# Kernel optimization log

Hardware: AMD Instinct MI355X
Metric: run time of the kernel (lower is better)

## Reference

```python
import jax, jax.numpy as jnp
import numpy as np

B = 64
HIST_LEN, PRED_HORIZON = 10, 10
H = W = 200
RES = 0.1
INIT_X_IDX, INIT_Y_IDX = 100.0, 160.0
FRONT_EDGE, BACK_EDGE = 3.89, 1.043
HALF_BOX = (FRONT_EDGE + BACK_EDGE) / 2.0
CENTER_SHIFT = HALF_BOX - BACK_EDGE          # mid-circle shift along box heading
FRONT_SHIFT = 2.0 * HALF_BOX - 2.0 * BACK_EDGE
EMBED, HIDDEN, CNN_OUT, CNN_CH = 64, 128, 1000, 32
SIGMA = 1.8
THETA = 0.0


def setup_inputs() -> dict:
    key = jax.random.key(0)
    ks = jax.random.split(key, 16)
    def rn(k, shape, scale=0.02):
        return jax.random.normal(k, shape, dtype=jnp.float32) * scale
    return {
        "img_feature": jax.random.normal(ks[0], (B, 12, H, W), dtype=jnp.float32),
        "hist_points": rn(ks[1], (B, HIST_LEN, 4), 1.0),
        "hist_points_step": rn(ks[2], (B, HIST_LEN, 4), 0.1),
        "ego_rendering_heading": jax.random.uniform(ks[3], (B, 1), dtype=jnp.float32, maxval=2.0 * np.pi),
        "comp_w": rn(ks[4], (3, 12, 3, 3)),
        "comp_b": jnp.zeros((3,), jnp.float32),
        "cnn_w": rn(ks[5], (CNN_CH, 3, 3, 3)),
        "cnn_b": jnp.zeros((CNN_CH,), jnp.float32),
        "cnn_fc_w": rn(ks[6], (CNN_OUT, CNN_CH)),
        "cnn_fc_b": jnp.zeros((CNN_OUT,), jnp.float32),
        "embed_w": rn(ks[7], (EMBED, 4)),
        "embed_b": jnp.zeros((EMBED,), jnp.float32),
        "h0": rn(ks[8], (1, HIDDEN)),
        "c0": rn(ks[9], (1, HIDDEN)),
        "w_ih": rn(ks[10], (4 * HIDDEN, EMBED)),
        "w_hh": rn(ks[11], (4 * HIDDEN, HIDDEN)),
        "b_ih": jnp.zeros((4 * HIDDEN,), jnp.float32),
        "b_hh": jnp.zeros((4 * HIDDEN,), jnp.float32),
        "out_w": rn(ks[12], (4, HIDDEN + CNN_OUT)),
        "out_b": jnp.zeros((4,), jnp.float32),
    }


def _conv(x, w, b, stride):
    y = jax.lax.conv_general_dilated(x, w, (stride, stride), 'SAME',
                                     dimension_numbers=('NCHW', 'OIHW', 'NCHW'))
    return y + b[None, :, None, None]


def _forward(img_feature, hist_points, hist_points_step, ego_rendering_heading,
             comp_w, comp_b, cnn_w, cnn_b, cnn_fc_w, cnn_fc_b,
             embed_w, embed_b, h0, c0, w_ih, w_hh, b_ih, b_hh, out_w, out_b):
    bsz = img_feature.shape[0]
    # CNN encoder: 12->3 compression conv, then backbone (stand-in for mobilenet_v2) -> 1000-dim
    z = _conv(img_feature, comp_w, comp_b, 1)
    z = jax.nn.relu(_conv(z, cnn_w, cnn_b, 2))
    z = z.mean(axis=(2, 3))                       # (B, CNN_CH) global avg pool
    img_emb = z @ cnn_fc_w.T + cnn_fc_b           # (B, 1000)

    def lstm_cell(e, h, c):                       # pytorch gate order i, f, g, o
        g = e @ w_ih.T + b_ih + h @ w_hh.T + b_hh
        i, f, gg, o = jnp.split(g, 4, axis=-1)
        c2 = jax.nn.sigmoid(f) * c + jax.nn.sigmoid(i) * jnp.tanh(gg)
        return jax.nn.sigmoid(o) * jnp.tanh(c2), c2

    def embed(step):
        return jax.nn.relu(step @ embed_w.T + embed_b)

    h = jnp.tile(h0, (bsz, 1))
    c = jnp.tile(c0, (bsz, 1))

    # warm up LSTM on history displacements (torch loop t = 1 .. HIST_LEN-1)
    def hist_step(carry, step_t):
        h, c = carry
        h, c = lstm_cell(embed(step_t), h, c)
        return (h, c), None
    (h, c), _ = jax.lax.scan(hist_step, (h, c),
                             jnp.swapaxes(hist_points_step[:, 1:HIST_LEN], 0, 1))

    def pred_step(carry, _):
        h, c, pose = carry
        step = jnp.concatenate([h, img_emb], axis=1) @ out_w.T + out_b
        pose = pose + step
        h, c = lstm_cell(embed(step), h, c)
        return (h, c, pose), pose
    _, poses = jax.lax.scan(pred_step, (h, c, hist_points[:, HIST_LEN - 1]),
                            None, length=PRED_HORIZON)
    pred_traj = jnp.swapaxes(poses, 0, 1)         # (B, T, 4) == torch pred_traj[:, 1:, :]

    # three-circle gaussian rasterization, vectorized over all timesteps
    ego = ego_rendering_heading.reshape(bsz)      # (B,)
    x, y, hd = pred_traj[..., 0], pred_traj[..., 1], pred_traj[..., 2]
    box_heading = -hd - ego[:, None]              # (B, T)
    ho = -(ego - np.pi / 2.0)                     # heading_offset, (B,)
    cos_ho, sin_ho = jnp.cos(ho)[:, None], jnp.sin(ho)[:, None]
    px = INIT_X_IDX + (x * cos_ho - y * sin_ho) / RES   # rear center in image idx
    py = INIT_Y_IDX - (x * sin_ho + y * cos_ho) / RES
    cos_bh, sin_bh = jnp.cos(box_heading), jnp.sin(box_heading)

    # idx_mesh built with meshgrid indexing='ij' over (W, H); image is square
    gx, gy = jnp.meshgrid(jnp.arange(W, dtype=jnp.float32),
                          jnp.arange(H, dtype=jnp.float32), indexing='ij')
    ct, st = np.cos(THETA), np.sin(THETA)
    ga = ct * ct / (2 * SIGMA ** 2) + st * st / (2 * SIGMA ** 2)
    gb = -np.sin(2 * THETA) / (4 * SIGMA ** 2) + np.sin(2 * THETA) / (4 * SIGMA ** 2)
    gc = st * st / (2 * SIGMA ** 2) + ct * ct / (2 * SIGMA ** 2)

    def gauss(shift):
        cx = px + shift / RES * cos_bh            # (B, T)
        cy = py - shift / RES * sin_bh
        dx = gx[None, None] - cx[..., None, None] # (B, T, H, W)
        dy = gy[None, None] - cy[..., None, None]
        return jnp.exp(-(ga * dx * dx + 2 * gb * dx * dy + gc * dy * dy))

    boxes = jnp.maximum(gauss(0.0), jnp.maximum(gauss(CENTER_SHIFT), gauss(FRONT_SHIFT)))
    pred_boxs = boxes[:, :, None]                 # (B, T, 1, H, W)
    return pred_traj, pred_boxs


def reference(img_feature, hist_points, hist_points_step, ego_rendering_heading,
              comp_w, comp_b, cnn_w, cnn_b, cnn_fc_w, cnn_fc_b,
              embed_w, embed_b, h0, c0, w_ih, w_hh, b_ih, b_hh, out_w, out_b):
    return _forward(img_feature, hist_points, hist_points_step, ego_rendering_heading,
                    comp_w, comp_b, cnn_w, cnn_b, cnn_fc_w, cnn_fc_b,
                    embed_w, embed_b, h0, c0, w_ih, w_hh, b_ih, b_hh, out_w, out_b)
```

## Files before the change

### kernel.cpp

```cpp
#include <hip/hip_runtime.h>
#include <math.h>

typedef _Float16 f16;
typedef f16 f16x2 __attribute__((ext_vector_type(2)));

__device__ __forceinline__ float dot2acc(f16x2 a, f16x2 b, float c){
#if __has_builtin(__builtin_amdgcn_fdot2)
  return __builtin_amdgcn_fdot2(a, b, c, false);
#else
  return c + (float)a[0]*(float)b[0] + (float)a[1]*(float)b[1];
#endif
}

__global__ __launch_bounds__(256) void k_convfused(
    const float* __restrict__ img, const float* __restrict__ cw, const float* __restrict__ cb,
    const float* __restrict__ w2, const float* __restrict__ b2,
    float* __restrict__ part){
  int b = blockIdx.y, ty = blockIdx.x;
  int oy0 = ty*5;
  int y1  = 2*oy0;
  int t = threadIdx.x;
  __shared__ float c1[3][11][204];

  if (t < 200){
    int x = t;
    const float* ib = img + (size_t)b*480000;
    float acc[3][11];
    #pragma unroll
    for (int oc=0;oc<3;++oc){
      float bz = cb[oc];
      #pragma unroll
      for (int r=0;r<11;++r) acc[oc][r] = bz;
    }
    bool xl = (x>0), xr = (x<199);
    for (int ci=0; ci<12; ++ci){
      const float* cbase = ib + ci*40000 + x;
      float vL[13], vM[13], vR[13];
      #pragma unroll
      for (int rr=0; rr<13; ++rr){
        int iy = y1-1+rr;
        bool rok = (unsigned)iy < 200u;
        const float* rp = cbase + iy*200;
        vL[rr] = (rok && xl) ? rp[-1] : 0.f;
        vM[rr] =  rok        ? rp[ 0] : 0.f;
        vR[rr] = (rok && xr) ? rp[ 1] : 0.f;
      }
      #pragma unroll
      for (int oc=0;oc<3;++oc){
        const float* wp = cw + oc*108 + ci*9;
        float w00=wp[0], w01=wp[1], w02=wp[2],
              w10=wp[3], w11=wp[4], w12=wp[5],
              w20=wp[6], w21=wp[7], w22=wp[8];
        #pragma unroll
        for (int r=0;r<11;++r){
          float s = acc[oc][r];
          s = fmaf(vL[r],   w00, s); s = fmaf(vM[r],   w01, s); s = fmaf(vR[r],   w02, s);
          s = fmaf(vL[r+1], w10, s); s = fmaf(vM[r+1], w11, s); s = fmaf(vR[r+1], w12, s);
          s = fmaf(vL[r+2], w20, s); s = fmaf(vM[r+2], w21, s); s = fmaf(vR[r+2], w22, s);
          acc[oc][r] = s;
        }
      }
    }
    #pragma unroll
    for (int oc=0;oc<3;++oc)
      #pragma unroll
      for (int r=0;r<11;++r)
        c1[oc][r][x] = acc[oc][r];
  }
  __syncthreads();

  float a2[32];
  #pragma unroll
  for (int co=0;co<32;++co) a2[co]=0.f;
  if (t < 250){
    #pragma unroll
    for (int e=0;e<2;++e){
      int px = t + 250*e;
      int q = px/100, ox = px - q*100;
      float v[27];
      #pragma unroll
      for (int ci=0;ci<3;++ci){
        #pragma unroll
        for (int ky=0;ky<3;++ky){
          int lr = 2*q+ky;
          bool rok = (y1 + lr) < 200;
          #pragma unroll
          for (int kx=0;kx<3;++kx){
            int ix = 2*ox+kx;
            v[ci*9+ky*3+kx] = (rok && ix<200) ? c1[ci][lr][ix] : 0.f;
          }
        }
      }
      #pragma unroll
      for (int co=0;co<32;++co){
        float s = b2[co];
        #pragma unroll
        for (int qq=0;qq<27;++qq) s = fmaf(v[qq], w2[co*27+qq], s);
        a2[co] += fmaxf(s, 0.f);
      }
    }
  }
  int lane = t&63, wv = t>>6;
  __shared__ float wred[4][32];
  #pragma unroll
  for (int co=0;co<32;++co){
    float s = a2[co];
    #pragma unroll
    for (int off=32; off; off>>=1) s += __shfl_down(s, off, 64);
    if (lane==0) wred[wv][co] = s;
  }
  __syncthreads();
  if (t < 32){
    float s = wred[0][t]+wred[1][t]+wred[2][t]+wred[3][t];
    part[(b*20+ty)*32 + t] = s;
  }
}

__global__ __launch_bounds__(256) void k_fc(const float* __restrict__ part,
    const float* __restrict__ fcw, const float* __restrict__ fcb,
    const float* __restrict__ ow, const float* __restrict__ ob,
    float* __restrict__ const4){
  int b = blockIdx.x, t = threadIdx.x, lane = t&63, wv = t>>6;
  __shared__ float z[32];
  __shared__ float wred[4][4];
  if (t < 32){
    float s = 0.f;
    #pragma unroll
    for (int p=0;p<20;++p) s += part[(b*20+p)*32 + t];
    z[t] = s * (1.f/10000.f);
  }
  __syncthreads();
  float cp0=0.f, cp1=0.f, cp2=0.f, cp3=0.f;
  for (int o = t; o < 1000; o += 256){
    float s = fcb[o];
    #pragma unroll
    for (int k=0;k<32;++k) s = fmaf(fcw[o*32+k], z[k], s);
    cp0 = fmaf(s, ow[0*1128+128+o], cp0);
    cp1 = fmaf(s, ow[1*1128+128+o], cp1);
    cp2 = fmaf(s, ow[2*1128+128+o], cp2);
    cp3 = fmaf(s, ow[3*1128+128+o], cp3);
  }
  #pragma unroll
  for (int off=32; off; off>>=1){
    cp0 += __shfl_down(cp0, off, 64);
    cp1 += __shfl_down(cp1, off, 64);
    cp2 += __shfl_down(cp2, off, 64);
    cp3 += __shfl_down(cp3, off, 64);
  }
  if (lane==0){ wred[wv][0]=cp0; wred[wv][1]=cp1; wred[wv][2]=cp2; wred[wv][3]=cp3; }
  __syncthreads();
  if (t < 4){
    float s = ob[t];
    #pragma unroll
    for (int q=0;q<4;++q) s += wred[q][t];
    const4[b*4+t] = s;
  }
}

__global__ __launch_bounds__(256) void k_lstm(
    const float* __restrict__ hist_pts, const float* __restrict__ hist_step,
    const float* __restrict__ emb_w, const float* __restrict__ emb_b,
    const float* __restrict__ h0, const float* __restrict__ c0,
    const float* __restrict__ w_ih, const float* __restrict__ w_hh,
    const float* __restrict__ b_ih, const float* __restrict__ b_hh,
    const float* __restrict__ out_w, const float* __restrict__ out_b,
    const float* __restrict__ const4, float* __restrict__ traj){
  int b = blockIdx.x; int t = threadIdx.x; int lane = t&63, wv = t>>6;
  int u  = (t<128) ? t       : t-128;
  int j1 = (t<128) ? t       : 128+u;
  int j2 = (t<128) ? 256+t   : 384+u;

  f16x2 w1[96], w2[96];
  {
    const float2* r1 = (const float2*)(w_ih + j1*64);
    const float2* r2 = (const float2*)(w_ih + j2*64);
    #pragma unroll
    for (int p=0;p<32;++p){
      float2 a = r1[p], c = r2[p];
      w1[p] = f16x2{(f16)a.x, (f16)a.y};
      w2[p] = f16x2{(f16)c.x, (f16)c.y};
    }
    const float2* q1 = (const float2*)(w_hh + j1*128);
    const float2* q2 = (const float2*)(w_hh + j2*128);
    #pragma unroll
    for (int p=0;p<64;++p){
      float2 a = q1[p], c = q2[p];
      w1[32+p] = f16x2{(f16)a.x, (f16)a.y};
      w2[32+p] = f16x2{(f16)c.x, (f16)c.y};
    }
  }
  float bias1 = b_ih[j1] + b_hh[j1];
  float bias2 = b_ih[j2] + b_hh[j2];

  __shared__ f16x2 xl[96];
  __shared__ float e_lds[64], h_lds[128], a_lds[128];
  __shared__ float step_lds[4], wred4[4];

  float c_reg = (t>=128) ? c0[u] : 0.f;
  if (t < 128) h_lds[t] = h0[t];

  auto cell = [&](){
    __syncthreads();
    if (t < 32)      xl[t]    = f16x2{(f16)e_lds[2*t],        (f16)e_lds[2*t+1]};
    else if (t < 96){ int p=t-32; xl[t] = f16x2{(f16)h_lds[2*p], (f16)h_lds[2*p+1]}; }
    __syncthreads();
    float acc1 = bias1, acc2 = bias2;
    #pragma unroll
    for (int cc=0; cc<12; ++cc){
      f16x2 xv[8];
      #pragma unroll
      for (int q=0;q<8;++q) xv[q] = xl[cc*8+q];
      #pragma unroll
      for (int q=0;q<8;++q){
        acc1 = dot2acc(w1[cc*8+q], xv[q], acc1);
        acc2 = dot2acc(w2[cc*8+q], xv[q], acc2);
      }
    }
    if (t < 128){
      float ig = 1.f/(1.f+expf(-acc1));
      float gg = tanhf(acc2);
      a_lds[t] = ig*gg;
    }
    __syncthreads();
    if (t >= 128){
      float ff = 1.f/(1.f+expf(-acc1));
      float oo = 1.f/(1.f+expf(-acc2));
      c_reg = ff*c_reg + a_lds[u];
      h_lds[u] = oo * tanhf(c_reg);
    }
  };

  for (int s=1; s<10; ++s){
    if (t < 64){
      const float* hp = hist_step + (size_t)(b*10+s)*4;
      float e = emb_b[t]
              + emb_w[t*4+0]*hp[0] + emb_w[t*4+1]*hp[1]
              + emb_w[t*4+2]*hp[2] + emb_w[t*4+3]*hp[3];
      e_lds[t] = fmaxf(e, 0.f);
    }
    cell();
  }

  float pose = (t<4) ? hist_pts[(size_t)(b*10+9)*4 + t] : 0.f;
  float cst  = (t<4) ? const4[b*4+t] : 0.f;
  for (int it=0; it<10; ++it){
    __syncthreads();
    {
      const float* owr = out_w + wv*1128;
      float p_ = owr[2*lane]*h_lds[2*lane] + owr[2*lane+1]*h_lds[2*lane+1];
      #pragma unroll
      for (int off=32; off; off>>=1) p_ += __shfl_down(p_, off, 64);
      if (lane==0) wred4[wv] = p_;
    }
    __syncthreads();
    if (t < 4){
      float st = wred4[t] + cst;
      pose += st;
      traj[(size_t)(b*10+it)*4 + t] = pose;
      step_lds[t] = st;
    }
    __syncthreads();
    if (it < 9){
      if (t < 64){
        float e = emb_b[t]
                + emb_w[t*4+0]*step_lds[0] + emb_w[t*4+1]*step_lds[1]
                + emb_w[t*4+2]*step_lds[2] + emb_w[t*4+3]*step_lds[3];
        e_lds[t] = fmaxf(e, 0.f);
      }
      cell();
    }
  }
}

__global__ __launch_bounds__(256) void k_raster(const float* __restrict__ traj,
    const float* __restrict__ ego, float* __restrict__ boxes){
  int img = blockIdx.y;
  int b = img / 10;
  __shared__ float ctr[6];
  if (threadIdx.x == 0){
    float x  = traj[img*4+0];
    float y  = traj[img*4+1];
    float hd = traj[img*4+2];
    float eg = ego[b];
    float ho = 1.5707963267948966f - eg;
    float sho, cho; __sincosf(ho, &sho, &cho);
    float pxc = 100.f + (x*cho - y*sho)*10.f;
    float pyc = 160.f - (x*sho + y*cho)*10.f;
    float bh  = -hd - eg;
    float sbh, cbh; __sincosf(bh, &sbh, &cbh);
    const float CSH = 14.235f;
    const float FSH = 28.47f;
    ctr[0] = pxc;             ctr[1] = pyc;
    ctr[2] = pxc + CSH*cbh;   ctr[3] = pyc - CSH*sbh;
    ctr[4] = pxc + FSH*cbh;   ctr[5] = pyc - FSH*sbh;
  }
  __syncthreads();
  int f4 = blockIdx.x*256 + threadIdx.x;
  if (f4 >= 10000) return;
  int p0 = f4*4;
  int i = p0 / 200;
  int j = p0 % 200;
  float fi = (float)i, fj = (float)j;
  float c0x=ctr[0], c0y=ctr[1], c1x=ctr[2], c1y=ctr[3], c2x=ctr[4], c2y=ctr[5];
  float dx0 = fi-c0x, dx1 = fi-c1x, dx2 = fi-c2x;
  float A0 = dx0*dx0, A1 = dx1*dx1, A2 = dx2*dx2;
  const float GA = 0.15432098765432098f;
  float r[4];
  #pragma unroll
  for (int l=0;l<4;++l){
    float dj = fj + (float)l;
    float dy0 = dj-c0y, dy1 = dj-c1y, dy2 = dj-c2y;
    float d0 = fmaf(dy0,dy0,A0);
    float d1 = fmaf(dy1,dy1,A1);
    float d2 = fmaf(dy2,dy2,A2);
    float m = fminf(d0, fminf(d1,d2));
    r[l] = __expf(-m*GA);
  }
  *(float4*)(boxes + (size_t)img*40000 + p0) = make_float4(r[0],r[1],r[2],r[3]);
}

extern "C" void kernel_launch(void* const* d_in, const int* in_sizes, int n_in,
                              void* d_out, int out_size, void* d_ws, size_t ws_size,
                              hipStream_t stream) {
  (void)in_sizes; (void)n_in; (void)d_ws; (void)ws_size; (void)out_size;
  const float* img = (const float*)d_in[0];
  const float* hp  = (const float*)d_in[1];
  const float* hps = (const float*)d_in[2];
  const float* ego = (const float*)d_in[3];
  const float* cw  = (const float*)d_in[4];
  const float* cb  = (const float*)d_in[5];
  const float* c2w = (const float*)d_in[6];
  const float* c2b = (const float*)d_in[7];
  const float* fcw = (const float*)d_in[8];
  const float* fcb = (const float*)d_in[9];
  const float* ew  = (const float*)d_in[10];
  const float* eb  = (const float*)d_in[11];
  const float* h0  = (const float*)d_in[12];
  const float* c0  = (const float*)d_in[13];
  const float* wih = (const float*)d_in[14];
  const float* whh = (const float*)d_in[15];
  const float* bih = (const float*)d_in[16];
  const float* bhh = (const float*)d_in[17];
  const float* ow  = (const float*)d_in[18];
  const float* ob  = (const float*)d_in[19];

  float* out  = (float*)d_out;
  float* traj = out;
  float* S    = out + 2560;
  float* part = S;
  float* cst4 = S + 40960;

  hipLaunchKernelGGL(k_convfused, dim3(20, 64), dim3(256), 0, stream,
                     img, cw, cb, c2w, c2b, part);
  hipLaunchKernelGGL(k_fc,    dim3(64),      dim3(256), 0, stream, part, fcw, fcb, ow, ob, cst4);
  hipLaunchKernelGGL(k_lstm,  dim3(64),      dim3(256), 0, stream,
                     hp, hps, ew, eb, h0, c0, wih, whh, bih, bhh, ow, ob, cst4, traj);
  hipLaunchKernelGGL(k_raster, dim3(40, 640), dim3(256), 0, stream, traj, ego, S);
}
```

Before: 155.3 us.

## Split fused conv into two kernels with 4x4 register tiling for first conv

The fused conv kernel is split into two kernels. The first conv computes the 12-to-3 channel conv with each thread owning a 4x4 output tile and using float4 loads, which removes the halo recomputation of the fused version where each block recomputed 11 rows for 10 needed. The result goes to a global scratch buffer in the output area. The second conv kernel reads that intermediate with vector loads, so it adds an extra global write and read plus one more launch in exchange for better reuse and less redundant work.

```diff
diff --git a/kernel.cpp b/kernel.cpp
--- a/kernel.cpp
+++ b/kernel.cpp
@@ -12,91 +12,107 @@
 #endif
 }
 
-__global__ __launch_bounds__(256) void k_convfused(
-    const float* __restrict__ img, const float* __restrict__ cw, const float* __restrict__ cb,
+__global__ __launch_bounds__(256) void k_conv1(const float* __restrict__ img,
+    const float* __restrict__ cw, const float* __restrict__ cb,
+    float* __restrict__ c1){
+  int b = blockIdx.y, ty = blockIdx.x;
+  int t = threadIdx.x;
+  if (t >= 250) return;
+  int cg = t % 50, rt = t / 50;
+  int x0 = cg*4;
+  int row0 = ty*20 + rt*4;
+  const float* ib = img + (size_t)b*480000;
+  float* ob = c1 + (size_t)b*120000;
+
+  float acc[3][4][4];
+  #pragma unroll
+  for (int oc=0;oc<3;++oc){
+    float bz = cb[oc];
+    #pragma unroll
+    for (int j=0;j<4;++j)
+      #pragma unroll
+      for (int c=0;c<4;++c) acc[oc][j][c] = bz;
+  }
+  bool xl = (x0>0), xr = (x0+4<200);
+  for (int ci=0; ci<12; ++ci){
+    const float* p = ib + ci*40000;
+    float vr[6][6];
+    #pragma unroll
+    for (int rr=0; rr<6; ++rr){
+      int iy = row0 - 1 + rr;
+      bool rok = (unsigned)iy < 200u;
+      const float* rp = p + iy*200 + x0;
+      float4 m = rok ? *(const float4*)rp : make_float4(0.f,0.f,0.f,0.f);
+      vr[rr][0] = (rok && xl) ? rp[-1] : 0.f;
+      vr[rr][1] = m.x; vr[rr][2] = m.y; vr[rr][3] = m.z; vr[rr][4] = m.w;
+      vr[rr][5] = (rok && xr) ? rp[4] : 0.f;
+    }
+    #pragma unroll
+    for (int oc=0;oc<3;++oc){
+      const float* wp = cw + oc*108 + ci*9;
+      float w00=wp[0], w01=wp[1], w02=wp[2],
+            w10=wp[3], w11=wp[4], w12=wp[5],
+            w20=wp[6], w21=wp[7], w22=wp[8];
+      #pragma unroll
+      for (int j=0;j<4;++j){
+        #pragma unroll
+        for (int c=0;c<4;++c){
+          float s = acc[oc][j][c];
+          s = fmaf(vr[j+0][c+0], w00, s); s = fmaf(vr[j+0][c+1], w01, s); s = fmaf(vr[j+0][c+2], w02, s);
+          s = fmaf(vr[j+1][c+0], w10, s); s = fmaf(vr[j+1][c+1], w11, s); s = fmaf(vr[j+1][c+2], w12, s);
+          s = fmaf(vr[j+2][c+0], w20, s); s = fmaf(vr[j+2][c+1], w21, s); s = fmaf(vr[j+2][c+2], w22, s);
+          acc[oc][j][c] = s;
+        }
+      }
+    }
+  }
+  #pragma unroll
+  for (int oc=0;oc<3;++oc)
+    #pragma unroll
+    for (int j=0;j<4;++j)
+      *(float4*)(ob + oc*40000 + (row0+j)*200 + x0) =
+        make_float4(acc[oc][j][0], acc[oc][j][1], acc[oc][j][2], acc[oc][j][3]);
+}
+
+__global__ __launch_bounds__(256) void k_conv2(const float* __restrict__ c1,
     const float* __restrict__ w2, const float* __restrict__ b2,
     float* __restrict__ part){
   int b = blockIdx.y, ty = blockIdx.x;
-  int oy0 = ty*5;
-  int y1  = 2*oy0;
   int t = threadIdx.x;
-  __shared__ float c1[3][11][204];
-
-  if (t < 200){
-    int x = t;
-    const float* ib = img + (size_t)b*480000;
-    float acc[3][11];
-    #pragma unroll
-    for (int oc=0;oc<3;++oc){
-      float bz = cb[oc];
-      #pragma unroll
-      for (int r=0;r<11;++r) acc[oc][r] = bz;
-    }
-    bool xl = (x>0), xr = (x<199);
-    for (int ci=0; ci<12; ++ci){
-      const float* cbase = ib + ci*40000 + x;
-      float vL[13], vM[13], vR[13];
-      #pragma unroll
-      for (int rr=0; rr<13; ++rr){
-        int iy = y1-1+rr;
-        bool rok = (unsigned)iy < 200u;
-        const float* rp = cbase + iy*200;
-        vL[rr] = (rok && xl) ? rp[-1] : 0.f;
-        vM[rr] =  rok        ? rp[ 0] : 0.f;
-        vR[rr] = (rok && xr) ? rp[ 1] : 0.f;
-      }
-      #pragma unroll
-      for (int oc=0;oc<3;++oc){
-        const float* wp = cw + oc*108 + ci*9;
-        float w00=wp[0], w01=wp[1], w02=wp[2],
-              w10=wp[3], w11=wp[4], w12=wp[5],
-              w20=wp[6], w21=wp[7], w22=wp[8];
-        #pragma unroll
-        for (int r=0;r<11;++r){
-          float s = acc[oc][r];
-          s = fmaf(vL[r],   w00, s); s = fmaf(vM[r],   w01, s); s = fmaf(vR[r],   w02, s);
-          s = fmaf(vL[r+1], w10, s); s = fmaf(vM[r+1], w11, s); s = fmaf(vR[r+1], w12, s);
-          s = fmaf(vL[r+2], w20, s); s = fmaf(vM[r+2], w21, s); s = fmaf(vR[r+2], w22, s);
-          acc[oc][r] = s;
-        }
-      }
-    }
-    #pragma unroll
-    for (int oc=0;oc<3;++oc)
-      #pragma unroll
-      for (int r=0;r<11;++r)
-        c1[oc][r][x] = acc[oc][r];
-  }
-  __syncthreads();
-
-  float a2[32];
-  #pragma unroll
-  for (int co=0;co<32;++co) a2[co]=0.f;
+  float acc[32];
+  #pragma unroll
+  for (int co=0;co<32;++co) acc[co]=0.f;
   if (t < 250){
-    #pragma unroll
-    for (int e=0;e<2;++e){
-      int px = t + 250*e;
-      int q = px/100, ox = px - q*100;
-      float v[27];
-      #pragma unroll
-      for (int ci=0;ci<3;++ci){
-        #pragma unroll
-        for (int ky=0;ky<3;++ky){
-          int lr = 2*q+ky;
-          bool rok = (y1 + lr) < 200;
-          #pragma unroll
-          for (int kx=0;kx<3;++kx){
-            int ix = 2*ox+kx;
-            v[ci*9+ky*3+kx] = (rok && ix<200) ? c1[ci][lr][ix] : 0.f;
-          }
-        }
-      }
+    int oy  = ty*5 + t/50;
+    int ox0 = (t%50)*2;
+    const float* cbs = c1 + (size_t)b*120000;
+    bool xl = (ox0>0);
+    float vr[3][3][5];
+    #pragma unroll
+    for (int ci=0;ci<3;++ci){
+      #pragma unroll
+      for (int ky=0;ky<3;++ky){
+        int iy = 2*oy + ky - 1;
+        bool rok = (iy >= 0);
+        const float* rp = cbs + ci*40000 + iy*200 + 2*ox0;
+        float4 m = rok ? *(const float4*)rp : make_float4(0.f,0.f,0.f,0.f);
+        vr[ci][ky][0] = (rok && xl) ? rp[-1] : 0.f;
+        vr[ci][ky][1] = m.x; vr[ci][ky][2] = m.y; vr[ci][ky][3] = m.z; vr[ci][ky][4] = m.w;
+      }
+    }
+    #pragma unroll
+    for (int c=0;c<2;++c){
       #pragma unroll
       for (int co=0;co<32;++co){
         float s = b2[co];
         #pragma unroll
-        for (int qq=0;qq<27;++qq) s = fmaf(v[qq], w2[co*27+qq], s);
-        a2[co] += fmaxf(s, 0.f);
+        for (int ci=0;ci<3;++ci)
+          #pragma unroll
+          for (int ky=0;ky<3;++ky)
+            #pragma unroll
+            for (int kx=0;kx<3;++kx)
+              s = fmaf(vr[ci][ky][2*c+kx], w2[co*27+ci*9+ky*3+kx], s);
+        acc[co] += fmaxf(s, 0.f);
       }
     }
   }
@@ -104,7 +120,7 @@
   __shared__ float wred[4][32];
   #pragma unroll
   for (int co=0;co<32;++co){
-    float s = a2[co];
+    float s = acc[co];
     #pragma unroll
     for (int off=32; off; off>>=1) s += __shfl_down(s, off, 64);
     if (lane==0) wred[wv][co] = s;
@@ -349,11 +365,12 @@
   float* S    = out + 2560;
   float* part = S;
   float* cst4 = S + 40960;
-
-  hipLaunchKernelGGL(k_convfused, dim3(20, 64), dim3(256), 0, stream,
-                     img, cw, cb, c2w, c2b, part);
-  hipLaunchKernelGGL(k_fc,    dim3(64),      dim3(256), 0, stream, part, fcw, fcb, ow, ob, cst4);
-  hipLaunchKernelGGL(k_lstm,  dim3(64),      dim3(256), 0, stream,
+  float* c1   = S + 50000;
+
+  hipLaunchKernelGGL(k_conv1, dim3(10, 64), dim3(256), 0, stream, img, cw, cb, c1);
+  hipLaunchKernelGGL(k_conv2, dim3(20, 64), dim3(256), 0, stream, c1, c2w, c2b, part);
+  hipLaunchKernelGGL(k_fc,    dim3(64),     dim3(256), 0, stream, part, fcw, fcb, ow, ob, cst4);
+  hipLaunchKernelGGL(k_lstm,  dim3(64),     dim3(256), 0, stream,
                      hp, hps, ew, eb, h0, c0, wih, whh, bih, bhh, ow, ob, cst4, traj);
   hipLaunchKernelGGL(k_raster, dim3(40, 640), dim3(256), 0, stream, traj, ego, S);
 }
```

After: 148.7 us. 1.04x faster.

## Stage conv input rows in LDS via direct global-to-LDS loads, remap threads

Applied to the files above, without the earlier changes.

The first compression conv now stages each input channel's 13 rows into shared memory using global_load_lds 16-byte transfers, with zero padding written for boundary tiles. Threads are remapped so each of 250 threads computes 4 adjacent output columns across 2-3 rows, reading float4 values from LDS instead of each thread issuing 39 scalar global loads per channel. This is meant to cut redundant global traffic and per-thread load latency and to use all 250 threads instead of 200. In exchange it adds two or three block-wide barriers per input channel, and the stride-2 indexing of the second conv is reworked to use the new z buffer layout.

```diff
diff --git a/kernel.cpp b/kernel.cpp
--- a/kernel.cpp
+++ b/kernel.cpp
@@ -17,93 +17,138 @@
     const float* __restrict__ w2, const float* __restrict__ b2,
     float* __restrict__ part){
   int b = blockIdx.y, ty = blockIdx.x;
-  int oy0 = ty*5;
-  int y1  = 2*oy0;
-  int t = threadIdx.x;
-  __shared__ float c1[3][11][204];
-
-  if (t < 200){
-    int x = t;
-    const float* ib = img + (size_t)b*480000;
-    float acc[3][11];
+  int t = threadIdx.x, lane = t & 63, wv = t >> 6;
+  int xr0 = 10*ty - 2;
+
+  __shared__ __align__(16) float stage_f[2608];
+  __shared__ __align__(16) float z_f[3*11*200];
+  __shared__ float wred[4][32];
+
+  int cg = t % 50, r = t / 50;
+  int NS = (r==0) ? 3 : 2;
+
+  float acc[3][3][4];
+  #pragma unroll
+  for (int s=0;s<3;++s)
     #pragma unroll
     for (int oc=0;oc<3;++oc){
       float bz = cb[oc];
       #pragma unroll
-      for (int r=0;r<11;++r) acc[oc][r] = bz;
-    }
-    bool xl = (x>0), xr = (x<199);
-    for (int ci=0; ci<12; ++ci){
-      const float* cbase = ib + ci*40000 + x;
-      float vL[13], vM[13], vR[13];
-      #pragma unroll
-      for (int rr=0; rr<13; ++rr){
-        int iy = y1-1+rr;
-        bool rok = (unsigned)iy < 200u;
-        const float* rp = cbase + iy*200;
-        vL[rr] = (rok && xl) ? rp[-1] : 0.f;
-        vM[rr] =  rok        ? rp[ 0] : 0.f;
-        vR[rr] = (rok && xr) ? rp[ 1] : 0.f;
-      }
-      #pragma unroll
-      for (int oc=0;oc<3;++oc){
-        const float* wp = cw + oc*108 + ci*9;
-        float w00=wp[0], w01=wp[1], w02=wp[2],
-              w10=wp[3], w11=wp[4], w12=wp[5],
-              w20=wp[6], w21=wp[7], w22=wp[8];
+      for (int c=0;c<4;++c) acc[s][oc][c] = bz;
+    }
+
+  const float* ibase = img + (size_t)b*480000;
+  bool boundary = (ty==0) | (ty==19);
+
+  for (int ci=0; ci<12; ++ci){
+    const float* cbase = ibase + ci*40000;
+    for (int s = wv; s < 11; s += 4){
+      int k = s*64 + lane;
+      if (k < 650){
+        int lr = k/50, cc = k - lr*50;
+        int rg = xr0 + lr; rg = rg < 0 ? 0 : (rg > 199 ? 199 : rg);
+        const float* g = cbase + rg*200 + cc*4;
+#if __has_builtin(__builtin_amdgcn_global_load_lds)
+        __builtin_amdgcn_global_load_lds(
+            (const __attribute__((address_space(1))) void*)g,
+            (__attribute__((address_space(3))) void*)&stage_f[k*4], 16, 0, 0);
+#else
+        *(float4*)&stage_f[k*4] = *(const float4*)g;
+#endif
+      }
+    }
+    __syncthreads();
+    if (boundary){
+      if (t < 200){
         #pragma unroll
-        for (int r=0;r<11;++r){
-          float s = acc[oc][r];
-          s = fmaf(vL[r],   w00, s); s = fmaf(vM[r],   w01, s); s = fmaf(vR[r],   w02, s);
-          s = fmaf(vL[r+1], w10, s); s = fmaf(vM[r+1], w11, s); s = fmaf(vR[r+1], w12, s);
-          s = fmaf(vL[r+2], w20, s); s = fmaf(vM[r+2], w21, s); s = fmaf(vR[r+2], w22, s);
-          acc[oc][r] = s;
+        for (int lr=0; lr<13; ++lr){
+          int rg = xr0 + lr;
+          if (rg < 0 || rg >= 200) stage_f[lr*200 + t] = 0.f;
         }
       }
-    }
-    #pragma unroll
-    for (int oc=0;oc<3;++oc)
-      #pragma unroll
-      for (int r=0;r<11;++r)
-        c1[oc][r][x] = acc[oc][r];
+      __syncthreads();
+    }
+    if (t < 250){
+      #pragma unroll
+      for (int s=0; s<3; ++s){
+        if (s >= NS) break;
+        int p = (s==2) ? 10 : r + 5*s;
+        #pragma unroll
+        for (int ky=0; ky<3; ++ky){
+          int xb = (p+ky)*200;
+          float4 vL = *(const float4*)&stage_f[xb + (cg ? 4*cg-4 : 0)];
+          float4 vM = *(const float4*)&stage_f[xb + 4*cg];
+          float4 vR = *(const float4*)&stage_f[xb + 4*cg + 4];
+          float v0 = cg ? vL.w : 0.f;
+          float v5 = (cg < 49) ? vR.x : 0.f;
+          float vv[6] = {v0, vM.x, vM.y, vM.z, vM.w, v5};
+          #pragma unroll
+          for (int oc=0; oc<3; ++oc){
+            const float* wp = cw + oc*108 + ci*9 + ky*3;
+            float w0 = wp[0], w1 = wp[1], w2_ = wp[2];
+            #pragma unroll
+            for (int c=0; c<4; ++c){
+              float ss = acc[s][oc][c];
+              ss = fmaf(vv[c],   w0,  ss);
+              ss = fmaf(vv[c+1], w1,  ss);
+              ss = fmaf(vv[c+2], w2_, ss);
+              acc[s][oc][c] = ss;
+            }
+          }
+        }
+      }
+    }
+    __syncthreads();
+  }
+
+  if (t < 250){
+    #pragma unroll
+    for (int s=0; s<3; ++s){
+      if (s >= NS) break;
+      int p = (s==2) ? 10 : r + 5*s;
+      bool zero = (ty==0) && (p==0);
+      #pragma unroll
+      for (int oc=0; oc<3; ++oc){
+        float4 w4 = zero ? make_float4(0.f,0.f,0.f,0.f)
+                         : make_float4(acc[s][oc][0], acc[s][oc][1], acc[s][oc][2], acc[s][oc][3]);
+        *(float4*)&z_f[(oc*11 + p)*200 + 4*cg] = w4;
+      }
+    }
   }
   __syncthreads();
 
   float a2[32];
   #pragma unroll
-  for (int co=0;co<32;++co) a2[co]=0.f;
+  for (int co=0; co<32; ++co) a2[co] = 0.f;
   if (t < 250){
     #pragma unroll
-    for (int e=0;e<2;++e){
-      int px = t + 250*e;
-      int q = px/100, ox = px - q*100;
-      float v[27];
-      #pragma unroll
-      for (int ci=0;ci<3;++ci){
+    for (int e=0; e<2; ++e){
+      int u = t + 250*e;
+      int oy = u/100, ox = u - oy*100;
+      float vtap[27];
+      int idx = 0;
+      #pragma unroll
+      for (int ci2=0; ci2<3; ++ci2)
         #pragma unroll
-        for (int ky=0;ky<3;++ky){
-          int lr = 2*q+ky;
-          bool rok = (y1 + lr) < 200;
+        for (int ky=0; ky<3; ++ky){
+          int pp = 2*oy + ky;
           #pragma unroll
-          for (int kx=0;kx<3;++kx){
-            int ix = 2*ox+kx;
-            v[ci*9+ky*3+kx] = (rok && ix<200) ? c1[ci][lr][ix] : 0.f;
+          for (int kx=0; kx<3; ++kx){
+            int zx = 2*ox + kx - 1;
+            vtap[idx++] = (zx >= 0) ? z_f[(ci2*11 + pp)*200 + zx] : 0.f;
           }
         }
-      }
-      #pragma unroll
-      for (int co=0;co<32;++co){
+      #pragma unroll
+      for (int co=0; co<32; ++co){
         float s = b2[co];
         #pragma unroll
-        for (int qq=0;qq<27;++qq) s = fmaf(v[qq], w2[co*27+qq], s);
+        for (int q=0; q<27; ++q) s = fmaf(vtap[q], w2[co*27+q], s);
         a2[co] += fmaxf(s, 0.f);
       }
     }
   }
-  int lane = t&63, wv = t>>6;
-  __shared__ float wred[4][32];
   #pragma unroll
-  for (int co=0;co<32;++co){
+  for (int co=0; co<32; ++co){
     float s = a2[co];
     #pragma unroll
     for (int off=32; off; off>>=1) s += __shfl_down(s, off, 64);
@@ -352,8 +397,8 @@
 
   hipLaunchKernelGGL(k_convfused, dim3(20, 64), dim3(256), 0, stream,
                      img, cw, cb, c2w, c2b, part);
-  hipLaunchKernelGGL(k_fc,    dim3(64),      dim3(256), 0, stream, part, fcw, fcb, ow, ob, cst4);
-  hipLaunchKernelGGL(k_lstm,  dim3(64),      dim3(256), 0, stream,
+  hipLaunchKernelGGL(k_fc,    dim3(64),     dim3(256), 0, stream, part, fcw, fcb, ow, ob, cst4);
+  hipLaunchKernelGGL(k_lstm,  dim3(64),     dim3(256), 0, stream,
                      hp, hps, ew, eb, h0, c0, wih, whh, bih, bhh, ow, ob, cst4, traj);
   hipLaunchKernelGGL(k_raster, dim3(40, 640), dim3(256), 0, stream, traj, ego, S);
 }
```

After: 163.2 us. 1.05x slower.
